# Optimization experiments

Measured on AMD Instinct MI355X. Metric: run time of the kernel, lower is better.

The kernel has to match this reference:

```python
import jax, jax.numpy as jnp
import numpy as np

B, T, V, E, H, N = 8, 128, 32000, 128, 256, 20
SHARPEN = 5.0
EPS = 1e-8  # torch cosine_similarity eps


def setup_inputs() -> dict:
    key = jax.random.key(0)
    ks = jax.random.split(key, 8)
    g = lambda k, shape, scale: (jax.random.normal(k, shape, dtype=jnp.float32) * scale)
    return {
        "x_ids": jax.random.randint(ks[0], (B, T), 0, V),
        "emb": g(ks[1], (V, E), 0.02),                 # nn.Embedding weight
        "W_i": g(ks[2], (H, E), E ** -0.5),            # rnn_i weight (no bias)
        "W_h": g(ks[3], (H, H), H ** -0.5),            # rnn_h weight
        "W_fc": g(ks[4], (V, 2 * H), (2 * H) ** -0.5), # fc -> vocab (softmaxed)
        "W_ops": g(ks[5], (3, 2 * H), (2 * H) ** -0.5),
        "W_choose": g(ks[6], (2, 2 * H), (2 * H) ** -0.5),
        "sharp": jnp.array([SHARPEN], dtype=jnp.float32),
    }


def _l2norm(x, eps=1e-12):
    # F.normalize(x, dim=-1)
    n = jnp.linalg.norm(x, axis=-1, keepdims=True)
    return x / jnp.maximum(n, eps)


def reference(x_ids, emb, W_i, W_h, W_fc, W_ops, W_choose, sharp):
    x = emb[x_ids]                                   # [B,T,E]
    # pre-normalize vocab rows for cosine-sim readout (clamped like torch)
    emb_cn = emb / jnp.maximum(jnp.linalg.norm(emb, axis=1, keepdims=True), EPS)
    sh = sharp[0]

    stack0 = jnp.full((B, N, E), 0.001, dtype=x.dtype)      # zero_offset + 0.001
    ptr0 = jnp.zeros((B, N), x.dtype).at[:, 0].set(1.0)     # pointer at slot 0
    h0 = jnp.zeros((B, H), x.dtype)

    def step(carry, xi):
        h, stack, ptr = carry
        ri = _l2norm(xi) @ W_i.T                     # rnn_i(normalize(x_t))
        h = jnp.tanh(ri + h @ W_h.T)
        hm = 1.0 - jax.nn.relu(h)
        hmod = jnp.concatenate([hm, hm], axis=1)     # [B,2H]
        # GumbelSoftmax(temp=1, hard=False) -> deterministic softmax (no noise)
        ops = jax.nn.softmax(hmod @ W_ops.T, axis=1)  # [B,3]
        push, pop, nop = ops[:, 0], ops[:, 1], ops[:, 2]
        # --- differentiable stack push/pop/nop ---
        pop_val = jnp.einsum('bn,bne->be', ptr, stack)      # soft read at pointer
        p_push = jnp.roll(ptr, 1, axis=1)
        p_pop = jnp.roll(ptr, -1, axis=1)
        new_ptr = push[:, None] * p_push + pop[:, None] * p_pop + nop[:, None] * ptr
        new_ptr = jnp.clip(new_ptr, EPS) ** sh              # sharpen
        new_ptr = new_ptr / jnp.sum(new_ptr, axis=1, keepdims=True)
        w = (push[:, None] * p_push)[:, :, None]            # write weight [B,N,1]
        new_stack = stack * (1.0 - w) + w * xi[:, None, :]
        # --- readout ---
        semantic = jax.nn.softmax(hmod @ W_fc.T, axis=1)    # [B,V]
        pv_n = pop_val / jnp.maximum(
            jnp.linalg.norm(pop_val, axis=1, keepdims=True), EPS)
        syntactic = pv_n @ emb_cn.T                          # cosine sim [B,V]
        choice = jax.nn.softmax(hmod @ W_choose.T, axis=1)   # [B,2]
        out = choice[:, 0:1] * semantic + choice[:, 1:2] * syntactic
        return (h, new_stack, new_ptr), out

    _, outs = jax.lax.scan(step, (h0, stack0, ptr0), jnp.swapaxes(x, 0, 1))
    return jnp.swapaxes(outs, 0, 1)  # [B,T,V]
```

## Files before the change

kernel.cpp:

```cpp
#include <hip/hip_runtime.h>
#include <hip/hip_bf16.h>
#include <stdint.h>

#define T_ 128
#define B_ 8
#define V_ 32000
#define E_ 128
#define H_ 256
#define N_ 20
#define M_ 1024
#define PIT 264
#define PIT2 136
#define NCH5 500

typedef __attribute__((ext_vector_type(8))) short short8;
typedef __attribute__((ext_vector_type(4))) float f32x4;
typedef unsigned short ushort;

static __device__ __forceinline__ ushort f2bf_u(float f) {
  __hip_bfloat16 h = __float2bfloat16(f);
  return *reinterpret_cast<ushort*>(&h);
}

__global__ void whb_k(const float* __restrict__ Wh, uint4* __restrict__ whb4) {
  int idx = blockIdx.x*256 + threadIdx.x;
  int k8 = idx >> 8, i = idx & 255;
  const float* s = Wh + i*H_ + k8*8;
  uint4 o;
  o.x = (uint32_t)f2bf_u(s[0]) | ((uint32_t)f2bf_u(s[1]) << 16);
  o.y = (uint32_t)f2bf_u(s[2]) | ((uint32_t)f2bf_u(s[3]) << 16);
  o.z = (uint32_t)f2bf_u(s[4]) | ((uint32_t)f2bf_u(s[5]) << 16);
  o.w = (uint32_t)f2bf_u(s[6]) | ((uint32_t)f2bf_u(s[7]) << 16);
  whb4[idx] = o;
}

__global__ void wit_k(const float* __restrict__ Wi, float* __restrict__ WiT) {
  int idx = blockIdx.x*256 + threadIdx.x;
  if (idx < H_*E_) {
    int i = idx >> 7, e = idx & (E_-1);
    WiT[e*H_ + i] = Wi[idx];
  }
}

__global__ __launch_bounds__(256) void ri_k(const int* __restrict__ x_ids,
    const float* __restrict__ emb, const float* __restrict__ WiT,
    float* __restrict__ RI)
{
  __shared__ float xn[E_];
  __shared__ float red[2];
  int r = blockIdx.x, tid = threadIdx.x;
  int id = x_ids[r];
  float v = 0.f;
  if (tid < E_) v = emb[id*E_ + tid];
  float ss = v*v;
  if (tid < E_) {
    #pragma unroll
    for (int off = 32; off >= 1; off >>= 1) ss += __shfl_xor(ss, off);
    if ((tid & 63) == 0) red[tid >> 6] = ss;
  }
  __syncthreads();
  float inv = 1.f / fmaxf(sqrtf(red[0] + red[1]), 1e-12f);
  if (tid < E_) xn[tid] = v*inv;
  __syncthreads();
  float s = 0.f;
  for (int e = 0; e < E_; ++e) s += xn[e]*WiT[e*H_ + tid];
  RI[r*H_ + tid] = s;
}

__global__ __launch_bounds__(1024) void chain_k(
    const uint4* __restrict__ whb4, const float* __restrict__ RI,
    float* __restrict__ HMf, ushort* __restrict__ HMb,
    const float* __restrict__ Wfc, const float* __restrict__ emb,
    ushort* __restrict__ Wfcb, ushort* __restrict__ embnb)
{
  __shared__ uint4 wlds[32*256];
  __shared__ __align__(16) float hbuf[2][H_];
  __shared__ float hred[3][H_];
  const int tid = threadIdx.x;

  if (blockIdx.x >= B_) {
    const int nb = gridDim.x - B_;
    const int bx = blockIdx.x - B_;
    for (long idx = (long)bx*1024 + tid; idx < (long)V_*H_; idx += (long)nb*1024) {
      int n = idx >> 8, k = idx & 255;
      Wfcb[idx] = f2bf_u(Wfc[(size_t)n*2*H_ + k] + Wfc[(size_t)n*2*H_ + H_ + k]);
    }
    const int wv = tid >> 6, l = tid & 63;
    for (int v = bx*16 + wv; v < V_; v += nb*16) {
      float e0 = emb[(size_t)v*E_ + l];
      float e1 = emb[(size_t)v*E_ + 64 + l];
      float ss = e0*e0 + e1*e1;
      #pragma unroll
      for (int off = 32; off >= 1; off >>= 1) ss += __shfl_xor(ss, off);
      float inv = 1.f / fmaxf(sqrtf(ss), 1e-8f);
      embnb[(size_t)v*E_ + l]      = f2bf_u(e0*inv);
      embnb[(size_t)v*E_ + 64 + l] = f2bf_u(e1*inv);
    }
    return;
  }

  const int b = blockIdx.x;
  const int q = tid >> 8, i = tid & 255;

  for (int m = tid; m < 32*256; m += 1024) wlds[m] = whb4[m];
  if (q == 0) hbuf[0][i] = 0.f;
  __syncthreads();
  float ri_c = (q == 0) ? RI[(size_t)b*T_*H_ + i] : 0.f;

  for (int t = 0; t < T_; ++t) {
    const int r = b*T_ + t;
    float ri_n = 0.f;
    if (q == 0 && t+1 < T_) ri_n = RI[(size_t)(r+1)*H_ + i];
    const float4* h4 = reinterpret_cast<const float4*>(hbuf[t & 1]);
    float p0 = 0.f, p1 = 0.f, p2 = 0.f, p3 = 0.f;
    #pragma unroll
    for (int j = 0; j < 8; ++j) {
      uint4 w = wlds[(q*8 + j)*256 + i];
      float4 ha = h4[q*16 + 2*j];
      float4 hb = h4[q*16 + 2*j + 1];
      p0 += __uint_as_float(w.x << 16)*ha.x + __uint_as_float(w.x & 0xffff0000u)*ha.y;
      p1 += __uint_as_float(w.y << 16)*ha.z + __uint_as_float(w.y & 0xffff0000u)*ha.w;
      p2 += __uint_as_float(w.z << 16)*hb.x + __uint_as_float(w.z & 0xffff0000u)*hb.y;
      p3 += __uint_as_float(w.w << 16)*hb.z + __uint_as_float(w.w & 0xffff0000u)*hb.w;
    }
    float p = (p0 + p1) + (p2 + p3);
    if (q) hred[q-1][i] = p;
    __syncthreads();
    if (q == 0) {
      float s = ri_c + p + hred[0][i] + hred[1][i] + hred[2][i];
      float hn = tanhf(s);
      hbuf[(t+1) & 1][i] = hn;
      float hm = 1.f - fmaxf(hn, 0.f);
      HMf[(size_t)r*H_ + i] = hm;
      HMb[(size_t)r*H_ + i] = f2bf_u(hm);
    }
    ri_c = ri_n;
    __syncthreads();
  }
}

__global__ __launch_bounds__(256) void stats6_k(const ushort* __restrict__ HMb,
    const ushort* __restrict__ Wfcb, const float* __restrict__ HMf,
    const float* __restrict__ W_ops, const float* __restrict__ W_ch,
    const float* __restrict__ sharp, const int* __restrict__ x_ids,
    const float* __restrict__ emb,
    float* __restrict__ SS, float* __restrict__ CH, float* __restrict__ PV,
    ushort* __restrict__ PVNb)
{
  __shared__ __align__(16) char smem[64*PIT*2];
  const int tid = threadIdx.x;
  const int wave = tid >> 6, lane = tid & 63;
  const int lr = lane & 15, g = lane >> 4;

  if (blockIdx.y == 0) {
    if (blockIdx.x >= B_) return;
    float*  ops_l = (float*)smem;
    float2* pw_l  = (float2*)(smem + 2048);
    int*    ids_l = (int*)(smem + 2048 + 20480);
    const int b = blockIdx.x;
    float wo[5][4];
    #pragma unroll
    for (int k = 0; k < 3; ++k)
      #pragma unroll
      for (int j = 0; j < 4; ++j)
        wo[k][j] = W_ops[k*2*H_ + 4*lane + j] + W_ops[k*2*H_ + H_ + 4*lane + j];
    #pragma unroll
    for (int k = 0; k < 2; ++k)
      #pragma unroll
      for (int j = 0; j < 4; ++j)
        wo[3+k][j] = W_ch[k*2*H_ + 4*lane + j] + W_ch[k*2*H_ + H_ + 4*lane + j];
    if (tid < T_) ids_l[tid] = x_ids[b*T_ + tid];
    for (int rl = wave*32; rl < wave*32 + 32; ++rl) {
      int R = b*T_ + rl;
      float4 hm4 = reinterpret_cast<const float4*>(HMf + (size_t)R*H_)[lane];
      float d0 = hm4.x*wo[0][0] + hm4.y*wo[0][1] + hm4.z*wo[0][2] + hm4.w*wo[0][3];
      float d1 = hm4.x*wo[1][0] + hm4.y*wo[1][1] + hm4.z*wo[1][2] + hm4.w*wo[1][3];
      float d2 = hm4.x*wo[2][0] + hm4.y*wo[2][1] + hm4.z*wo[2][2] + hm4.w*wo[2][3];
      float d3 = hm4.x*wo[3][0] + hm4.y*wo[3][1] + hm4.z*wo[3][2] + hm4.w*wo[3][3];
      float d4 = hm4.x*wo[4][0] + hm4.y*wo[4][1] + hm4.z*wo[4][2] + hm4.w*wo[4][3];
      #pragma unroll
      for (int off = 32; off >= 1; off >>= 1) {
        d0 += __shfl_xor(d0, off); d1 += __shfl_xor(d1, off); d2 += __shfl_xor(d2, off);
        d3 += __shfl_xor(d3, off); d4 += __shfl_xor(d4, off);
      }
      if (lane == 0) {
        float mx = fmaxf(d0, fmaxf(d1, d2));
        float e0 = expf(d0-mx), e1 = expf(d1-mx), e2 = expf(d2-mx);
        float oi = 1.f/(e0+e1+e2);
        ops_l[rl*4+0] = e0*oi; ops_l[rl*4+1] = e1*oi; ops_l[rl*4+2] = e2*oi;
        float cm = fmaxf(d3, d4);
        float f0 = expf(d3-cm), f1 = expf(d4-cm);
        float ci = 1.f/(f0+f1);
        CH[R*2] = f0*ci; CH[R*2+1] = f1*ci;
      }
    }
    __syncthreads();
    if (tid < 64) {
      const float sh = sharp[0];
      float ptr = (tid == 0) ? 1.f : 0.f;
      const int lp = (tid + N_ - 1) % N_, ln = (tid + 1) % N_;
      for (int t = 0; t < T_; ++t) {
        float push = ops_l[t*4+0], pop = ops_l[t*4+1], nop = ops_l[t*4+2];
        float pp = __shfl(ptr, lp);
        float po = __shfl(ptr, ln);
        float wgt = push*pp;
        float raw = wgt + pop*po + nop*ptr;
        float np = 0.f;
        if (tid < N_) np = exp2f(sh * log2f(fmaxf(raw, 1e-8f)));
        float ssum = np;
        #pragma unroll
        for (int off = 1; off < 32; off <<= 1) ssum += __shfl_xor(ssum, off);
        if (tid < N_) {
          pw_l[t*N_ + tid] = make_float2(ptr, wgt);
          ptr = np / ssum;
        }
      }
    }
    __syncthreads();
    if (tid < E_) {
      const int e = tid;
      float stck[N_];
      #pragma unroll
      for (int n = 0; n < N_; ++n) stck[n] = 0.001f;
      float xi_c = emb[(size_t)ids_l[0]*E_ + e];
      for (int t = 0; t < T_; ++t) {
        float xi_n = (t+1 < T_) ? emb[(size_t)ids_l[t+1]*E_ + e] : 0.f;
        float pv = 0.f;
        #pragma unroll
        for (int n = 0; n < N_; ++n) {
          float2 pw = pw_l[t*N_ + n];
          pv += pw.x * stck[n];
          stck[n] += pw.y * (xi_c - stck[n]);
        }
        PV[(size_t)(b*T_ + t)*E_ + e] = pv;
        xi_c = xi_n;
      }
    }
    __threadfence_block();
    __syncthreads();
    for (int rl = wave*32; rl < wave*32 + 32; ++rl) {
      int R = b*T_ + rl;
      float a = PV[(size_t)R*E_ + lane];
      float c = PV[(size_t)R*E_ + 64 + lane];
      float ss = a*a + c*c;
      #pragma unroll
      for (int off = 32; off >= 1; off >>= 1) ss += __shfl_xor(ss, off);
      float inv = 1.f / fmaxf(sqrtf(ss), 1e-8f);
      PVNb[(size_t)R*E_ + lane]      = f2bf_u(a*inv);
      PVNb[(size_t)R*E_ + 64 + lane] = f2bf_u(c*inv);
    }
    return;
  }

  ushort* Bs = (ushort*)smem;
  const int Cb = blockIdx.x*64;
  {
    const uint4* srcB = (const uint4*)(Wfcb + (size_t)Cb*H_);
    #pragma unroll
    for (int it = 0; it < 8; ++it) {
      int idx = it*256 + tid, row = idx >> 5, c = idx & 31;
      *(uint4*)&Bs[row*PIT + c*8] = srcB[row*32 + c];
    }
  }
  const int Rw = (blockIdx.y - 1)*256 + wave*64;
  __syncthreads();
  f32x4 acc[4][4] = {};
  #pragma unroll
  for (int ks = 0; ks < 8; ++ks) {
    short8 a0 = *(const short8*)(HMb + (size_t)(Rw + 0*16 + lr)*H_ + ks*32 + g*8);
    short8 a1 = *(const short8*)(HMb + (size_t)(Rw + 1*16 + lr)*H_ + ks*32 + g*8);
    short8 a2 = *(const short8*)(HMb + (size_t)(Rw + 2*16 + lr)*H_ + ks*32 + g*8);
    short8 a3 = *(const short8*)(HMb + (size_t)(Rw + 3*16 + lr)*H_ + ks*32 + g*8);
    short8 b0 = *(const short8*)(&Bs[(0*16 + lr)*PIT + ks*32 + g*8]);
    short8 b1 = *(const short8*)(&Bs[(1*16 + lr)*PIT + ks*32 + g*8]);
    short8 b2 = *(const short8*)(&Bs[(2*16 + lr)*PIT + ks*32 + g*8]);
    short8 b3 = *(const short8*)(&Bs[(3*16 + lr)*PIT + ks*32 + g*8]);
    #define MF(mi, av) \
      acc[mi][0] = __builtin_amdgcn_mfma_f32_16x16x32_bf16(av, b0, acc[mi][0], 0, 0, 0); \
      acc[mi][1] = __builtin_amdgcn_mfma_f32_16x16x32_bf16(av, b1, acc[mi][1], 0, 0, 0); \
      acc[mi][2] = __builtin_amdgcn_mfma_f32_16x16x32_bf16(av, b2, acc[mi][2], 0, 0, 0); \
      acc[mi][3] = __builtin_amdgcn_mfma_f32_16x16x32_bf16(av, b3, acc[mi][3], 0, 0, 0);
    MF(0, a0) MF(1, a1) MF(2, a2) MF(3, a3)
    #undef MF
  }
  #pragma unroll
  for (int mi = 0; mi < 4; ++mi)
    #pragma unroll
    for (int r = 0; r < 4; ++r) {
      float s = expf(acc[mi][0][r]) + expf(acc[mi][1][r])
              + expf(acc[mi][2][r]) + expf(acc[mi][3][r]);
      #pragma unroll
      for (int off = 1; off < 16; off <<= 1) s += __shfl_xor(s, off);
      if (lr == 0) SS[(size_t)blockIdx.x*M_ + (Rw + mi*16 + g*4 + r)] = s;
    }
}

__global__ void reduce5_k(const float* __restrict__ SS, float* __restrict__ MS) {
  int row = blockIdx.x, l = threadIdx.x;
  float s = 0.f;
  for (int c = l; c < NCH5; c += 64) s += SS[(size_t)c*M_ + row];
  #pragma unroll
  for (int off = 32; off >= 1; off >>= 1) s += __shfl_xor(s, off);
  if (l == 0) MS[row] = 1.f/s;
}

__global__ __launch_bounds__(256) void final6_k(const ushort* __restrict__ HMb,
    const ushort* __restrict__ Wfcb, const ushort* __restrict__ PVNb,
    const ushort* __restrict__ embnb, const float* __restrict__ MS,
    const float* __restrict__ CH, float* __restrict__ out)
{
  __shared__ __align__(16) ushort Bs[64*PIT];
  const int tid = threadIdx.x;
  const int Cb = blockIdx.x*64;
  const int wave = tid >> 6, lane = tid & 63;
  const int lr = lane & 15, g = lane >> 4;
  const int Rw = blockIdx.y*256 + wave*64;

  {
    const uint4* srcB = (const uint4*)(Wfcb + (size_t)Cb*H_);
    #pragma unroll
    for (int it = 0; it < 8; ++it) {
      int idx = it*256 + tid, row = idx >> 5, c = idx & 31;
      *(uint4*)&Bs[row*PIT + c*8] = srcB[row*32 + c];
    }
  }
  __syncthreads();
  f32x4 accL[4][4] = {};
  #pragma unroll
  for (int ks = 0; ks < 8; ++ks) {
    short8 a0 = *(const short8*)(HMb + (size_t)(Rw + 0*16 + lr)*H_ + ks*32 + g*8);
    short8 a1 = *(const short8*)(HMb + (size_t)(Rw + 1*16 + lr)*H_ + ks*32 + g*8);
    short8 a2 = *(const short8*)(HMb + (size_t)(Rw + 2*16 + lr)*H_ + ks*32 + g*8);
    short8 a3 = *(const short8*)(HMb + (size_t)(Rw + 3*16 + lr)*H_ + ks*32 + g*8);
    short8 b0 = *(const short8*)(&Bs[(0*16 + lr)*PIT + ks*32 + g*8]);
    short8 b1 = *(const short8*)(&Bs[(1*16 + lr)*PIT + ks*32 + g*8]);
    short8 b2 = *(const short8*)(&Bs[(2*16 + lr)*PIT + ks*32 + g*8]);
    short8 b3 = *(const short8*)(&Bs[(3*16 + lr)*PIT + ks*32 + g*8]);
    #define MFL(mi, av) \
      accL[mi][0] = __builtin_amdgcn_mfma_f32_16x16x32_bf16(av, b0, accL[mi][0], 0, 0, 0); \
      accL[mi][1] = __builtin_amdgcn_mfma_f32_16x16x32_bf16(av, b1, accL[mi][1], 0, 0, 0); \
      accL[mi][2] = __builtin_amdgcn_mfma_f32_16x16x32_bf16(av, b2, accL[mi][2], 0, 0, 0); \
      accL[mi][3] = __builtin_amdgcn_mfma_f32_16x16x32_bf16(av, b3, accL[mi][3], 0, 0, 0);
    MFL(0, a0) MFL(1, a1) MFL(2, a2) MFL(3, a3)
    #undef MFL
  }
  __syncthreads();

  {
    const uint4* srcB = (const uint4*)(embnb + (size_t)Cb*E_);
    #pragma unroll
    for (int it = 0; it < 4; ++it) {
      int idx = it*256 + tid, row = idx >> 4, c = idx & 15;
      *(uint4*)&Bs[row*PIT2 + c*8] = srcB[row*16 + c];
    }
  }
  __syncthreads();
  f32x4 accS[4][4] = {};
  #pragma unroll
  for (int ks = 0; ks < 4; ++ks) {
    short8 a0 = *(const short8*)(PVNb + (size_t)(Rw + 0*16 + lr)*E_ + ks*32 + g*8);
    short8 a1 = *(const short8*)(PVNb + (size_t)(Rw + 1*16 + lr)*E_ + ks*32 + g*8);
    short8 a2 = *(const short8*)(PVNb + (size_t)(Rw + 2*16 + lr)*E_ + ks*32 + g*8);
    short8 a3 = *(const short8*)(PVNb + (size_t)(Rw + 3*16 + lr)*E_ + ks*32 + g*8);
    short8 b0 = *(const short8*)(&Bs[(0*16 + lr)*PIT2 + ks*32 + g*8]);
    short8 b1 = *(const short8*)(&Bs[(1*16 + lr)*PIT2 + ks*32 + g*8]);
    short8 b2 = *(const short8*)(&Bs[(2*16 + lr)*PIT2 + ks*32 + g*8]);
    short8 b3 = *(const short8*)(&Bs[(3*16 + lr)*PIT2 + ks*32 + g*8]);
    #define MFS(mi, av) \
      accS[mi][0] = __builtin_amdgcn_mfma_f32_16x16x32_bf16(av, b0, accS[mi][0], 0, 0, 0); \
      accS[mi][1] = __builtin_amdgcn_mfma_f32_16x16x32_bf16(av, b1, accS[mi][1], 0, 0, 0); \
      accS[mi][2] = __builtin_amdgcn_mfma_f32_16x16x32_bf16(av, b2, accS[mi][2], 0, 0, 0); \
      accS[mi][3] = __builtin_amdgcn_mfma_f32_16x16x32_bf16(av, b3, accS[mi][3], 0, 0, 0);
    MFS(0, a0) MFS(1, a1) MFS(2, a2) MFS(3, a3)
    #undef MFS
  }

  #pragma unroll
  for (int mi = 0; mi < 4; ++mi)
    #pragma unroll
    for (int r = 0; r < 4; ++r) {
      int row = Rw + mi*16 + g*4 + r;
      float Si = MS[row];
      float c0 = CH[row*2], c1 = CH[row*2+1];
      size_t base = (size_t)row*V_ + Cb + lr;
      #pragma unroll
      for (int nj = 0; nj < 4; ++nj)
        out[base + nj*16] = c0*expf(accL[mi][nj][r])*Si + c1*accS[mi][nj][r];
    }
}

extern "C" void kernel_launch(void* const* d_in, const int* in_sizes, int n_in,
                              void* d_out, int out_size, void* d_ws, size_t ws_size,
                              hipStream_t stream) {
  const int*   x_ids = (const int*)d_in[0];
  const float* emb   = (const float*)d_in[1];
  const float* W_i   = (const float*)d_in[2];
  const float* W_h   = (const float*)d_in[3];
  const float* W_fc  = (const float*)d_in[4];
  const float* W_ops = (const float*)d_in[5];
  const float* W_ch  = (const float*)d_in[6];
  const float* sharp = (const float*)d_in[7];
  float* out = (float*)d_out;

  float* ws    = (float*)d_ws;
  uint4*  whb4 = (uint4*)ws;
  float*  WiT  = ws + 65536;
  float*  RI   = WiT + 32768;
  float*  CH   = RI + 262144;
  float*  MS   = CH + 2048;
  float*  SS   = MS + 1024;
  float*  HMf  = SS + 512000;
  float*  PV   = HMf + 262144;
  float*  fend = PV + 131072;
  ushort* HMb   = (ushort*)fend;
  ushort* PVNb  = HMb + 262144;
  ushort* Wfcb  = PVNb + 131072;
  ushort* embnb = Wfcb + 8192000;

  whb_k  <<<32, 256, 0, stream>>>(W_h, whb4);
  wit_k  <<<(H_*E_ + 255)/256, 256, 0, stream>>>(W_i, WiT);
  ri_k   <<<M_, 256, 0, stream>>>(x_ids, emb, WiT, RI);
  chain_k<<<248, 1024, 0, stream>>>(whb4, RI, HMf, HMb, W_fc, emb, Wfcb, embnb);
  stats6_k<<<dim3(NCH5, 5), 256, 0, stream>>>(HMb, Wfcb, HMf, W_ops, W_ch, sharp,
                                              x_ids, emb, SS, CH, PV, PVNb);
  reduce5_k<<<M_, 64, 0, stream>>>(SS, MS);
  final6_k<<<dim3(NCH5, M_/256), 256, 0, stream>>>(HMb, Wfcb, PVNb, embnb, MS, CH, out);
}
```

Baseline: 383.7 us.

## Reuse staged W_fc and emb tiles across all row tiles per block

The stats and final GEMM kernels now loop over all four 256-row tiles inside one block instead of spreading them across the grid's y dimension. Each block stages its W_fc and normalized-emb column tile in shared memory once, which cuts repeated global loads of the vocab weights. The final kernel keeps both B tiles resident at once, removing a sync and reload, and the A fragments are preloaded into registers per tile. The two prep kernels are also merged into one launch. The trade-off is fewer blocks (500 instead of 2000) and higher register pressure from the preloaded A arrays, which could lower occupancy and latency hiding.

Result: slower. 420.8 us (+9.7%).

```diff
diff --git a/kernel.cpp b/kernel.cpp
--- a/kernel.cpp
+++ b/kernel.cpp
@@ -22,23 +22,24 @@
   return *reinterpret_cast<ushort*>(&h);
 }
 
-__global__ void whb_k(const float* __restrict__ Wh, uint4* __restrict__ whb4) {
-  int idx = blockIdx.x*256 + threadIdx.x;
-  int k8 = idx >> 8, i = idx & 255;
-  const float* s = Wh + i*H_ + k8*8;
-  uint4 o;
-  o.x = (uint32_t)f2bf_u(s[0]) | ((uint32_t)f2bf_u(s[1]) << 16);
-  o.y = (uint32_t)f2bf_u(s[2]) | ((uint32_t)f2bf_u(s[3]) << 16);
-  o.z = (uint32_t)f2bf_u(s[4]) | ((uint32_t)f2bf_u(s[5]) << 16);
-  o.w = (uint32_t)f2bf_u(s[6]) | ((uint32_t)f2bf_u(s[7]) << 16);
-  whb4[idx] = o;
-}
-
-__global__ void wit_k(const float* __restrict__ Wi, float* __restrict__ WiT) {
-  int idx = blockIdx.x*256 + threadIdx.x;
-  if (idx < H_*E_) {
-    int i = idx >> 7, e = idx & (E_-1);
-    WiT[e*H_ + i] = Wi[idx];
+__global__ void prep_k(const float* __restrict__ Wh, uint4* __restrict__ whb4,
+                       const float* __restrict__ Wi, float* __restrict__ WiT) {
+  if (blockIdx.x < 32) {
+    int idx = blockIdx.x*256 + threadIdx.x;
+    int k8 = idx >> 8, i = idx & 255;
+    const float* s = Wh + i*H_ + k8*8;
+    uint4 o;
+    o.x = (uint32_t)f2bf_u(s[0]) | ((uint32_t)f2bf_u(s[1]) << 16);
+    o.y = (uint32_t)f2bf_u(s[2]) | ((uint32_t)f2bf_u(s[3]) << 16);
+    o.z = (uint32_t)f2bf_u(s[4]) | ((uint32_t)f2bf_u(s[5]) << 16);
+    o.w = (uint32_t)f2bf_u(s[6]) | ((uint32_t)f2bf_u(s[7]) << 16);
+    whb4[idx] = o;
+  } else {
+    int idx = (blockIdx.x - 32)*256 + threadIdx.x;
+    if (idx < H_*E_) {
+      int i = idx >> 7, e = idx & (E_-1);
+      WiT[e*H_ + i] = Wi[idx];
+    }
   }
 }
 
@@ -139,7 +140,7 @@
   }
 }
 
-__global__ __launch_bounds__(256) void stats6_k(const ushort* __restrict__ HMb,
+__global__ __launch_bounds__(256) void stats7_k(const ushort* __restrict__ HMb,
     const ushort* __restrict__ Wfcb, const float* __restrict__ HMf,
     const float* __restrict__ W_ops, const float* __restrict__ W_ch,
     const float* __restrict__ sharp, const int* __restrict__ x_ids,
@@ -262,37 +263,41 @@
       *(uint4*)&Bs[row*PIT + c*8] = srcB[row*32 + c];
     }
   }
-  const int Rw = (blockIdx.y - 1)*256 + wave*64;
   __syncthreads();
-  f32x4 acc[4][4] = {};
-  #pragma unroll
-  for (int ks = 0; ks < 8; ++ks) {
-    short8 a0 = *(const short8*)(HMb + (size_t)(Rw + 0*16 + lr)*H_ + ks*32 + g*8);
-    short8 a1 = *(const short8*)(HMb + (size_t)(Rw + 1*16 + lr)*H_ + ks*32 + g*8);
-    short8 a2 = *(const short8*)(HMb + (size_t)(Rw + 2*16 + lr)*H_ + ks*32 + g*8);
-    short8 a3 = *(const short8*)(HMb + (size_t)(Rw + 3*16 + lr)*H_ + ks*32 + g*8);
-    short8 b0 = *(const short8*)(&Bs[(0*16 + lr)*PIT + ks*32 + g*8]);
-    short8 b1 = *(const short8*)(&Bs[(1*16 + lr)*PIT + ks*32 + g*8]);
-    short8 b2 = *(const short8*)(&Bs[(2*16 + lr)*PIT + ks*32 + g*8]);
-    short8 b3 = *(const short8*)(&Bs[(3*16 + lr)*PIT + ks*32 + g*8]);
-    #define MF(mi, av) \
-      acc[mi][0] = __builtin_amdgcn_mfma_f32_16x16x32_bf16(av, b0, acc[mi][0], 0, 0, 0); \
-      acc[mi][1] = __builtin_amdgcn_mfma_f32_16x16x32_bf16(av, b1, acc[mi][1], 0, 0, 0); \
-      acc[mi][2] = __builtin_amdgcn_mfma_f32_16x16x32_bf16(av, b2, acc[mi][2], 0, 0, 0); \
-      acc[mi][3] = __builtin_amdgcn_mfma_f32_16x16x32_bf16(av, b3, acc[mi][3], 0, 0, 0);
-    MF(0, a0) MF(1, a1) MF(2, a2) MF(3, a3)
-    #undef MF
-  }
-  #pragma unroll
-  for (int mi = 0; mi < 4; ++mi)
-    #pragma unroll
-    for (int r = 0; r < 4; ++r) {
-      float s = expf(acc[mi][0][r]) + expf(acc[mi][1][r])
-              + expf(acc[mi][2][r]) + expf(acc[mi][3][r]);
-      #pragma unroll
-      for (int off = 1; off < 16; off <<= 1) s += __shfl_xor(s, off);
-      if (lr == 0) SS[(size_t)blockIdx.x*M_ + (Rw + mi*16 + g*4 + r)] = s;
-    }
+  for (int mt = 0; mt < 4; ++mt) {
+    const int Rw = mt*256 + wave*64;
+    short8 a[4][8];
+    #pragma unroll
+    for (int mi = 0; mi < 4; ++mi)
+      #pragma unroll
+      for (int ks = 0; ks < 8; ++ks)
+        a[mi][ks] = *(const short8*)(HMb + (size_t)(Rw + mi*16 + lr)*H_ + ks*32 + g*8);
+    f32x4 acc[4][4] = {};
+    #pragma unroll
+    for (int ks = 0; ks < 8; ++ks) {
+      short8 b0 = *(const short8*)(&Bs[(0*16 + lr)*PIT + ks*32 + g*8]);
+      short8 b1 = *(const short8*)(&Bs[(1*16 + lr)*PIT + ks*32 + g*8]);
+      short8 b2 = *(const short8*)(&Bs[(2*16 + lr)*PIT + ks*32 + g*8]);
+      short8 b3 = *(const short8*)(&Bs[(3*16 + lr)*PIT + ks*32 + g*8]);
+      #define MF(mi) \
+        acc[mi][0] = __builtin_amdgcn_mfma_f32_16x16x32_bf16(a[mi][ks], b0, acc[mi][0], 0, 0, 0); \
+        acc[mi][1] = __builtin_amdgcn_mfma_f32_16x16x32_bf16(a[mi][ks], b1, acc[mi][1], 0, 0, 0); \
+        acc[mi][2] = __builtin_amdgcn_mfma_f32_16x16x32_bf16(a[mi][ks], b2, acc[mi][2], 0, 0, 0); \
+        acc[mi][3] = __builtin_amdgcn_mfma_f32_16x16x32_bf16(a[mi][ks], b3, acc[mi][3], 0, 0, 0);
+      MF(0) MF(1) MF(2) MF(3)
+      #undef MF
+    }
+    #pragma unroll
+    for (int mi = 0; mi < 4; ++mi)
+      #pragma unroll
+      for (int r = 0; r < 4; ++r) {
+        float s = expf(acc[mi][0][r]) + expf(acc[mi][1][r])
+                + expf(acc[mi][2][r]) + expf(acc[mi][3][r]);
+        #pragma unroll
+        for (int off = 1; off < 16; off <<= 1) s += __shfl_xor(s, off);
+        if (lr == 0) SS[(size_t)blockIdx.x*M_ + (Rw + mi*16 + g*4 + r)] = s;
+      }
+  }
 }
 
 __global__ void reduce5_k(const float* __restrict__ SS, float* __restrict__ MS) {
@@ -304,89 +309,95 @@
   if (l == 0) MS[row] = 1.f/s;
 }
 
-__global__ __launch_bounds__(256) void final6_k(const ushort* __restrict__ HMb,
+__global__ __launch_bounds__(256) void final7_k(const ushort* __restrict__ HMb,
     const ushort* __restrict__ Wfcb, const ushort* __restrict__ PVNb,
     const ushort* __restrict__ embnb, const float* __restrict__ MS,
     const float* __restrict__ CH, float* __restrict__ out)
 {
-  __shared__ __align__(16) ushort Bs[64*PIT];
+  __shared__ __align__(16) ushort Bs1[64*PIT];
+  __shared__ __align__(16) ushort Bs2[64*PIT2];
   const int tid = threadIdx.x;
   const int Cb = blockIdx.x*64;
   const int wave = tid >> 6, lane = tid & 63;
   const int lr = lane & 15, g = lane >> 4;
-  const int Rw = blockIdx.y*256 + wave*64;
 
   {
     const uint4* srcB = (const uint4*)(Wfcb + (size_t)Cb*H_);
     #pragma unroll
     for (int it = 0; it < 8; ++it) {
       int idx = it*256 + tid, row = idx >> 5, c = idx & 31;
-      *(uint4*)&Bs[row*PIT + c*8] = srcB[row*32 + c];
-    }
-  }
-  __syncthreads();
-  f32x4 accL[4][4] = {};
-  #pragma unroll
-  for (int ks = 0; ks < 8; ++ks) {
-    short8 a0 = *(const short8*)(HMb + (size_t)(Rw + 0*16 + lr)*H_ + ks*32 + g*8);
-    short8 a1 = *(const short8*)(HMb + (size_t)(Rw + 1*16 + lr)*H_ + ks*32 + g*8);
-    short8 a2 = *(const short8*)(HMb + (size_t)(Rw + 2*16 + lr)*H_ + ks*32 + g*8);
-    short8 a3 = *(const short8*)(HMb + (size_t)(Rw + 3*16 + lr)*H_ + ks*32 + g*8);
-    short8 b0 = *(const short8*)(&Bs[(0*16 + lr)*PIT + ks*32 + g*8]);
-    short8 b1 = *(const short8*)(&Bs[(1*16 + lr)*PIT + ks*32 + g*8]);
-    short8 b2 = *(const short8*)(&Bs[(2*16 + lr)*PIT + ks*32 + g*8]);
-    short8 b3 = *(const short8*)(&Bs[(3*16 + lr)*PIT + ks*32 + g*8]);
-    #define MFL(mi, av) \
-      accL[mi][0] = __builtin_amdgcn_mfma_f32_16x16x32_bf16(av, b0, accL[mi][0], 0, 0, 0); \
-      accL[mi][1] = __builtin_amdgcn_mfma_f32_16x16x32_bf16(av, b1, accL[mi][1], 0, 0, 0); \
-      accL[mi][2] = __builtin_amdgcn_mfma_f32_16x16x32_bf16(av, b2, accL[mi][2], 0, 0, 0); \
-      accL[mi][3] = __builtin_amdgcn_mfma_f32_16x16x32_bf16(av, b3, accL[mi][3], 0, 0, 0);
-    MFL(0, a0) MFL(1, a1) MFL(2, a2) MFL(3, a3)
-    #undef MFL
-  }
-  __syncthreads();
-
-  {
-    const uint4* srcB = (const uint4*)(embnb + (size_t)Cb*E_);
+      *(uint4*)&Bs1[row*PIT + c*8] = srcB[row*32 + c];
+    }
+    const uint4* srcS = (const uint4*)(embnb + (size_t)Cb*E_);
     #pragma unroll
     for (int it = 0; it < 4; ++it) {
       int idx = it*256 + tid, row = idx >> 4, c = idx & 15;
-      *(uint4*)&Bs[row*PIT2 + c*8] = srcB[row*16 + c];
+      *(uint4*)&Bs2[row*PIT2 + c*8] = srcS[row*16 + c];
     }
   }
   __syncthreads();
-  f32x4 accS[4][4] = {};
-  #pragma unroll
-  for (int ks = 0; ks < 4; ++ks) {
-    short8 a0 = *(const short8*)(PVNb + (size_t)(Rw + 0*16 + lr)*E_ + ks*32 + g*8);
-    short8 a1 = *(const short8*)(PVNb + (size_t)(Rw + 1*16 + lr)*E_ + ks*32 + g*8);
-    short8 a2 = *(const short8*)(PVNb + (size_t)(Rw + 2*16 + lr)*E_ + ks*32 + g*8);
-    short8 a3 = *(const short8*)(PVNb + (size_t)(Rw + 3*16 + lr)*E_ + ks*32 + g*8);
-    short8 b0 = *(const short8*)(&Bs[(0*16 + lr)*PIT2 + ks*32 + g*8]);
-    short8 b1 = *(const short8*)(&Bs[(1*16 + lr)*PIT2 + ks*32 + g*8]);
-    short8 b2 = *(const short8*)(&Bs[(2*16 + lr)*PIT2 + ks*32 + g*8]);
-    short8 b3 = *(const short8*)(&Bs[(3*16 + lr)*PIT2 + ks*32 + g*8]);
-    #define MFS(mi, av) \
-      accS[mi][0] = __builtin_amdgcn_mfma_f32_16x16x32_bf16(av, b0, accS[mi][0], 0, 0, 0); \
-      accS[mi][1] = __builtin_amdgcn_mfma_f32_16x16x32_bf16(av, b1, accS[mi][1], 0, 0, 0); \
-      accS[mi][2] = __builtin_amdgcn_mfma_f32_16x16x32_bf16(av, b2, accS[mi][2], 0, 0, 0); \
-      accS[mi][3] = __builtin_amdgcn_mfma_f32_16x16x32_bf16(av, b3, accS[mi][3], 0, 0, 0);
-    MFS(0, a0) MFS(1, a1) MFS(2, a2) MFS(3, a3)
-    #undef MFS
-  }
-
-  #pragma unroll
-  for (int mi = 0; mi < 4; ++mi)
-    #pragma unroll
-    for (int r = 0; r < 4; ++r) {
-      int row = Rw + mi*16 + g*4 + r;
-      float Si = MS[row];
-      float c0 = CH[row*2], c1 = CH[row*2+1];
-      size_t base = (size_t)row*V_ + Cb + lr;
-      #pragma unroll
-      for (int nj = 0; nj < 4; ++nj)
-        out[base + nj*16] = c0*expf(accL[mi][nj][r])*Si + c1*accS[mi][nj][r];
-    }
+
+  for (int mt = 0; mt < 4; ++mt) {
+    const int Rw = mt*256 + wave*64;
+    f32x4 accL[4][4] = {};
+    {
+      short8 a[4][8];
+      #pragma unroll
+      for (int mi = 0; mi < 4; ++mi)
+        #pragma unroll
+        for (int ks = 0; ks < 8; ++ks)
+          a[mi][ks] = *(const short8*)(HMb + (size_t)(Rw + mi*16 + lr)*H_ + ks*32 + g*8);
+      #pragma unroll
+      for (int ks = 0; ks < 8; ++ks) {
+        short8 b0 = *(const short8*)(&Bs1[(0*16 + lr)*PIT + ks*32 + g*8]);
+        short8 b1 = *(const short8*)(&Bs1[(1*16 + lr)*PIT + ks*32 + g*8]);
+        short8 b2 = *(const short8*)(&Bs1[(2*16 + lr)*PIT + ks*32 + g*8]);
+        short8 b3 = *(const short8*)(&Bs1[(3*16 + lr)*PIT + ks*32 + g*8]);
+        #define MFL(mi) \
+          accL[mi][0] = __builtin_amdgcn_mfma_f32_16x16x32_bf16(a[mi][ks], b0, accL[mi][0], 0, 0, 0); \
+          accL[mi][1] = __builtin_amdgcn_mfma_f32_16x16x32_bf16(a[mi][ks], b1, accL[mi][1], 0, 0, 0); \
+          accL[mi][2] = __builtin_amdgcn_mfma_f32_16x16x32_bf16(a[mi][ks], b2, accL[mi][2], 0, 0, 0); \
+          accL[mi][3] = __builtin_amdgcn_mfma_f32_16x16x32_bf16(a[mi][ks], b3, accL[mi][3], 0, 0, 0);
+        MFL(0) MFL(1) MFL(2) MFL(3)
+        #undef MFL
+      }
+    }
+    f32x4 accS[4][4] = {};
+    {
+      short8 a2[4][4];
+      #pragma unroll
+      for (int mi = 0; mi < 4; ++mi)
+        #pragma unroll
+        for (int ks = 0; ks < 4; ++ks)
+          a2[mi][ks] = *(const short8*)(PVNb + (size_t)(Rw + mi*16 + lr)*E_ + ks*32 + g*8);
+      #pragma unroll
+      for (int ks = 0; ks < 4; ++ks) {
+        short8 b0 = *(const short8*)(&Bs2[(0*16 + lr)*PIT2 + ks*32 + g*8]);
+        short8 b1 = *(const short8*)(&Bs2[(1*16 + lr)*PIT2 + ks*32 + g*8]);
+        short8 b2 = *(const short8*)(&Bs2[(2*16 + lr)*PIT2 + ks*32 + g*8]);
+        short8 b3 = *(const short8*)(&Bs2[(3*16 + lr)*PIT2 + ks*32 + g*8]);
+        #define MFS(mi) \
+          accS[mi][0] = __builtin_amdgcn_mfma_f32_16x16x32_bf16(a2[mi][ks], b0, accS[mi][0], 0, 0, 0); \
+          accS[mi][1] = __builtin_amdgcn_mfma_f32_16x16x32_bf16(a2[mi][ks], b1, accS[mi][1], 0, 0, 0); \
+          accS[mi][2] = __builtin_amdgcn_mfma_f32_16x16x32_bf16(a2[mi][ks], b2, accS[mi][2], 0, 0, 0); \
+          accS[mi][3] = __builtin_amdgcn_mfma_f32_16x16x32_bf16(a2[mi][ks], b3, accS[mi][3], 0, 0, 0);
+        MFS(0) MFS(1) MFS(2) MFS(3)
+        #undef MFS
+      }
+    }
+    #pragma unroll
+    for (int mi = 0; mi < 4; ++mi)
+      #pragma unroll
+      for (int r = 0; r < 4; ++r) {
+        int row = Rw + mi*16 + g*4 + r;
+        float Si = MS[row];
+        float c0 = CH[row*2], c1 = CH[row*2+1];
+        size_t base = (size_t)row*V_ + Cb + lr;
+        #pragma unroll
+        for (int nj = 0; nj < 4; ++nj)
+          out[base + nj*16] = c0*expf(accL[mi][nj][r])*Si + c1*accS[mi][nj][r];
+      }
+  }
 }
 
 extern "C" void kernel_launch(void* const* d_in, const int* in_sizes, int n_in,
@@ -417,12 +428,11 @@
   ushort* Wfcb  = PVNb + 131072;
   ushort* embnb = Wfcb + 8192000;
 
-  whb_k  <<<32, 256, 0, stream>>>(W_h, whb4);
-  wit_k  <<<(H_*E_ + 255)/256, 256, 0, stream>>>(W_i, WiT);
+  prep_k <<<160, 256, 0, stream>>>(W_h, whb4, W_i, WiT);
   ri_k   <<<M_, 256, 0, stream>>>(x_ids, emb, WiT, RI);
   chain_k<<<248, 1024, 0, stream>>>(whb4, RI, HMf, HMb, W_fc, emb, Wfcb, embnb);
-  stats6_k<<<dim3(NCH5, 5), 256, 0, stream>>>(HMb, Wfcb, HMf, W_ops, W_ch, sharp,
+  stats7_k<<<dim3(NCH5, 2), 256, 0, stream>>>(HMb, Wfcb, HMf, W_ops, W_ch, sharp,
                                               x_ids, emb, SS, CH, PV, PVNb);
   reduce5_k<<<M_, 64, 0, stream>>>(SS, MS);
-  final6_k<<<dim3(NCH5, M_/256), 256, 0, stream>>>(HMb, Wfcb, PVNb, embnb, MS, CH, out);
-}
+  final7_k<<<NCH5, 256, 0, stream>>>(HMb, Wfcb, PVNb, embnb, MS, CH, out);
+}
```
